# Kernel optimization log

Measured on AMD Instinct MI355X. Metric: run time of the kernel, lower is better.

Reference implementation:

```python
import jax, jax.numpy as jnp
import numpy as np


def setup_inputs() -> dict:
    key = jax.random.key(0)
    ks = jax.random.split(key, 8)
    B, C, H, W = 8, 256, 64, 64
    Cqk = C // 8
    x = jax.random.normal(ks[0], (B, C, H, W), dtype=jnp.float32)
    # 1x1 conv weights, stored as [out_ch, in_ch] (kernel is 1x1)
    Wq = jax.random.normal(ks[1], (Cqk, C), dtype=jnp.float32) * 0.02
    bq = jnp.zeros((Cqk,), dtype=jnp.float32)
    Wk = jax.random.normal(ks[2], (Cqk, C), dtype=jnp.float32) * 0.02
    bk = jnp.zeros((Cqk,), dtype=jnp.float32)
    Wv = jax.random.normal(ks[3], (C, C), dtype=jnp.float32) * 0.02
    bv = jnp.zeros((C,), dtype=jnp.float32)
    # gamma initialized to zero in the module; use small nonzero so grads flow through attention path meaningfully
    gamma = jnp.asarray([0.5], dtype=jnp.float32)
    return {"x": x, "Wq": Wq, "bq": bq, "Wk": Wk, "bk": bk, "Wv": Wv, "bv": bv, "gamma": gamma}


def reference(x, Wq, bq, Wk, bk, Wv, bv, gamma):
    B, C, H, W = x.shape
    N = H * W
    xf = x.reshape(B, C, N)  # [B, C, N]
    # 1x1 convs == channel-wise matmuls
    q = jnp.einsum('oc,bcn->bno', Wq, xf) + bq  # [B, N, Cqk]
    k = jnp.einsum('oc,bcn->bon', Wk, xf) + bk[None, :, None]  # [B, Cqk, N]
    v = jnp.einsum('oc,bcn->bon', Wv, xf) + bv[None, :, None]  # [B, C, N]
    energy = jnp.einsum('bnd,bdm->bnm', q, k)  # [B, N, N], unscaled as in original
    attn = jax.nn.softmax(energy, axis=-1)
    out = jnp.einsum('bcm,bnm->bcn', v, attn)  # out[:, :, n] = sum_m v[:, :, m] * attn[n, m]
    out = out.reshape(B, C, H, W)
    return gamma[0] * out + x
```

## Files before the change

### kernel.cpp

```cpp
#include <hip/hip_runtime.h>
#include <hip/hip_bf16.h>

#define NB 8
#define CH 256
#define NN 4096
#define CQK 32
#define LOG2E 1.4426950408889634f

typedef __attribute__((ext_vector_type(4))) float f32x4;
typedef __attribute__((ext_vector_type(8))) short bf16x8;
typedef unsigned short u16;

static __device__ __forceinline__ u16 f2bf(float f) {
  unsigned int u = __float_as_uint(f);
  unsigned int r = (u + 0x7fffu + ((u >> 16) & 1u)) >> 16;
  return (u16)r;
}

__global__ void prep_weights(const float* __restrict__ Wq, const float* __restrict__ bq,
                             const float* __restrict__ Wk, const float* __restrict__ bk,
                             const float* __restrict__ Wv,
                             u16* __restrict__ Wqkf, u16* __restrict__ Wvf,
                             float* __restrict__ bqk) {
  int i = blockIdx.x * 256 + threadIdx.x;
  int o = i >> 8, c = i & 255;
  int kk = c >> 5, g2 = (c >> 3) & 3, j = c & 7;
  if (o < 64) {
    float wv = (o < 32) ? Wq[o * 256 + c] * LOG2E : Wk[(o - 32) * 256 + c];
    Wqkf[((((o >> 4) * 8 + kk) * 4 + g2) * 16 + (o & 15)) * 8 + j] = f2bf(wv);
  }
  Wvf[((((o >> 4) * 8 + kk) * 4 + g2) * 16 + (o & 15)) * 8 + j] = f2bf(Wv[i]);
  if (i < 64) bqk[i] = (i < 32) ? bq[i] * LOG2E : bk[i - 32];
}

__global__ __launch_bounds__(256, 2) void fused_proj(
    const float* __restrict__ x, const u16* __restrict__ Wqkf,
    const u16* __restrict__ Wvf, const float* __restrict__ bqk,
    const float* __restrict__ bv,
    u16* __restrict__ qbuf, u16* __restrict__ kbuf, u16* __restrict__ vbuf) {
  __shared__ __align__(128) char xt[64 * 512];
  const int b = blockIdx.y, n0 = blockIdx.x * 64;
  const int tid = threadIdx.x, w = tid >> 6, l = tid & 63, g = l >> 4, lr = l & 15;
  const f32x4 fzero = {0.f, 0.f, 0.f, 0.f};

  {
    const int nl = l, cl = w;
    const float* xp = x + (size_t)b * CH * NN + n0 + nl;
    char* xrow = xt + nl * 512;
    const int swz = (nl & 15) << 4;
#pragma unroll
    for (int p = 0; p < 32; ++p) {
      const int c = p * 8 + cl * 2;
      float f0 = xp[(size_t)c * NN], f1 = xp[(size_t)(c + 1) * NN];
      unsigned int pk = (unsigned int)f2bf(f0) | ((unsigned int)f2bf(f1) << 16);
      *(unsigned int*)(xrow + ((c * 2) ^ swz)) = pk;
    }
  }
  __syncthreads();

  const int aswz = lr << 4;

  {
    f32x4 acc[4];
#pragma unroll
    for (int ct = 0; ct < 4; ++ct) acc[ct] = fzero;
#pragma unroll
    for (int kk = 0; kk < 8; ++kk) {
      bf16x8 af = *(const bf16x8*)(xt + (w * 16 + lr) * 512 + ((kk * 64 + g * 16) ^ aswz));
#pragma unroll
      for (int ct = 0; ct < 4; ++ct) {
        bf16x8 bf = *(const bf16x8*)(Wqkf + (size_t)(((ct * 8 + kk) * 4 + g) * 16 + lr) * 8);
        acc[ct] = __builtin_amdgcn_mfma_f32_16x16x32_bf16(af, bf, acc[ct], 0, 0, 0);
      }
    }
#pragma unroll
    for (int ct = 0; ct < 4; ++ct) {
      const int col = ct * 16 + lr;
      const float bc = bqk[col];
#pragma unroll
      for (int r = 0; r < 4; ++r) {
        const int row = n0 + w * 16 + g * 4 + r;
        u16 h = f2bf(acc[ct][r] + bc);
        if (col < 32) qbuf[((size_t)(b * NN + row)) * 32 + col] = h;
        else          kbuf[((size_t)(b * NN + row)) * 32 + (col - 32)] = h;
      }
    }
  }

  {
    f32x4 vacc[4][4];
#pragma unroll
    for (int ct = 0; ct < 4; ++ct)
#pragma unroll
      for (int mt = 0; mt < 4; ++mt) vacc[ct][mt] = fzero;
#pragma unroll
    for (int kk = 0; kk < 8; ++kk) {
      bf16x8 bfm[4];
#pragma unroll
      for (int mt = 0; mt < 4; ++mt)
        bfm[mt] = *(const bf16x8*)(xt + (mt * 16 + lr) * 512 + ((kk * 64 + g * 16) ^ aswz));
#pragma unroll
      for (int ct = 0; ct < 4; ++ct) {
        bf16x8 af = *(const bf16x8*)(Wvf + (size_t)((((w * 4 + ct) * 8 + kk) * 4 + g) * 16 + lr) * 8);
#pragma unroll
        for (int mt = 0; mt < 4; ++mt)
          vacc[ct][mt] = __builtin_amdgcn_mfma_f32_16x16x32_bf16(af, bfm[mt], vacc[ct][mt], 0, 0, 0);
      }
    }
#pragma unroll
    for (int ct = 0; ct < 4; ++ct) {
#pragma unroll
      for (int mt = 0; mt < 4; ++mt) {
        const int m = n0 + mt * 16 + lr;
#pragma unroll
        for (int r = 0; r < 4; ++r) {
          const int ch = w * 64 + ct * 16 + g * 4 + r;
          vbuf[((size_t)(b * 128 + (m >> 5)) * 256 + ch) * 32 + (m & 31)] = f2bf(vacc[ct][mt][r] + bv[ch]);
        }
      }
    }
  }
}

#define KLOAD(t, sub) (*(const bf16x8*)(kp + (size_t)((((t) & 63) * 64) + (sub) * 16) * 32))
#define VLOAD(mg, ct) (*(const bf16x8*)(vp + (size_t)((mg) & 127) * 8192 + (ct) * 512))

#define EXPP(S, PW, MASK) {                                                                   \
  float e0 = __builtin_amdgcn_exp2f(S[0]);                                                    \
  float e1 = __builtin_amdgcn_exp2f(S[1]);                                                    \
  float e2 = __builtin_amdgcn_exp2f(S[2]);                                                    \
  float e3 = __builtin_amdgcn_exp2f(S[3]);                                                    \
  lsum += (MASK) * ((e0 + e1) + (e2 + e3));                                                   \
  PW.x = __builtin_amdgcn_perm(__float_as_uint(e1) + 0x8000u, __float_as_uint(e0) + 0x8000u, 0x07060302u); \
  PW.y = __builtin_amdgcn_perm(__float_as_uint(e3) + 0x8000u, __float_as_uint(e2) + 0x8000u, 0x07060302u); \
}

#define PBAR() do {                                  \
  __builtin_amdgcn_sched_barrier(0);                 \
  asm volatile("s_waitcnt lgkmcnt(0)");              \
  __builtin_amdgcn_s_barrier();                      \
  __builtin_amdgcn_sched_barrier(0);                 \
} while (0)

#define PVPHASE(BUF, V0, V1, V2, V3) {                                                        \
  const char* prb = (const char*)Pb + (BUF) * 16384;                                          \
  char* pdst = (char*)Pb + ((BUF) ^ 1) * 16384 + prow * 128;                                  \
  *(uint2*)(pdst + ((0 * 32 + g * 8) ^ wswz)) = pw0;                                          \
  *(uint2*)(pdst + ((1 * 32 + g * 8) ^ wswz)) = pw1;                                          \
  *(uint2*)(pdst + ((2 * 32 + g * 8) ^ wswz)) = pw2;                                          \
  *(uint2*)(pdst + ((3 * 32 + g * 8) ^ wswz)) = pw3;                                          \
  __builtin_amdgcn_s_setprio(1);                                                              \
  _Pragma("unroll")                                                                           \
  for (int nt = 0; nt < 8; ++nt) {                                                            \
    const int row = nt * 16 + lr;                                                             \
    const int rs = (row & 7) << 4;                                                            \
    bf16x8 pa0 = *(const bf16x8*)(prb + row * 128 + ((g * 16) ^ rs));                         \
    bf16x8 pa1 = *(const bf16x8*)(prb + row * 128 + ((64 + g * 16) ^ rs));                    \
    oacc[nt][0] = __builtin_amdgcn_mfma_f32_16x16x32_bf16(V0, pa0, oacc[nt][0], 0, 0, 0);     \
    oacc[nt][1] = __builtin_amdgcn_mfma_f32_16x16x32_bf16(V1, pa0, oacc[nt][1], 0, 0, 0);     \
    oacc[nt][0] = __builtin_amdgcn_mfma_f32_16x16x32_bf16(V2, pa1, oacc[nt][0], 0, 0, 0);     \
    oacc[nt][1] = __builtin_amdgcn_mfma_f32_16x16x32_bf16(V3, pa1, oacc[nt][1], 0, 0, 0);     \
  }                                                                                           \
  __builtin_amdgcn_s_setprio(0);                                                              \
}

__global__ __launch_bounds__(512, 2) void attn_fused(
    const u16* __restrict__ qb, const u16* __restrict__ kbuf,
    const u16* __restrict__ vbuf, const float* __restrict__ x,
    const float* __restrict__ gamma_p, float* __restrict__ out) {
  __shared__ __align__(128) char Pb[2][128 * 128];
  __shared__ float lpart[8][16];

  const int b = blockIdx.x;
  const int n0 = blockIdx.y * 128;
  const int tid = threadIdx.x, w = tid >> 6, l = tid & 63, g = l >> 4, lr = l & 15;
  const float gamma0 = gamma_p[0];
  const f32x4 fzero = {0.f, 0.f, 0.f, 0.f};

  bf16x8 qf = *(const bf16x8*)(qb + ((size_t)b * NN + n0 + w * 16 + lr) * 32 + g * 8);

  const u16* kp = kbuf + (size_t)b * (NN * 32) + (size_t)lr * 32 + g * 8;
  const u16* vp = vbuf + (size_t)b * 1048576 + (size_t)(w * 32 + lr) * 32 + g * 8;

  f32x4 oacc[8][2];
#pragma unroll
  for (int nt = 0; nt < 8; ++nt)
#pragma unroll
    for (int ct = 0; ct < 2; ++ct) oacc[nt][ct] = fzero;
  float lsum = 0.f;

  const int prow = w * 16 + lr;
  const int wswz = (prow & 7) << 4;

  bf16x8 kA0 = KLOAD(0, 0), kA1 = KLOAD(0, 1), kA2 = KLOAD(0, 2), kA3 = KLOAD(0, 3);
  bf16x8 vA0 = VLOAD(0, 0), vA1 = VLOAD(0, 1), vA2 = VLOAD(1, 0), vA3 = VLOAD(1, 1);
  bf16x8 kB0 = KLOAD(1, 0), kB1 = KLOAD(1, 1), kB2 = KLOAD(1, 2), kB3 = KLOAD(1, 3);
  bf16x8 vB0, vB1, vB2, vB3;
  uint2 pw0, pw1, pw2, pw3;
  {
    f32x4 s0 = __builtin_amdgcn_mfma_f32_16x16x32_bf16(kA0, qf, fzero, 0, 0, 0);
    f32x4 s1 = __builtin_amdgcn_mfma_f32_16x16x32_bf16(kA1, qf, fzero, 0, 0, 0);
    f32x4 s2 = __builtin_amdgcn_mfma_f32_16x16x32_bf16(kA2, qf, fzero, 0, 0, 0);
    f32x4 s3 = __builtin_amdgcn_mfma_f32_16x16x32_bf16(kA3, qf, fzero, 0, 0, 0);
    EXPP(s0, pw0, 1.0f); EXPP(s1, pw1, 1.0f); EXPP(s2, pw2, 1.0f); EXPP(s3, pw3, 1.0f);
    char* pdst = (char*)Pb + prow * 128;
    *(uint2*)(pdst + ((0 * 32 + g * 8) ^ wswz)) = pw0;
    *(uint2*)(pdst + ((1 * 32 + g * 8) ^ wswz)) = pw1;
    *(uint2*)(pdst + ((2 * 32 + g * 8) ^ wswz)) = pw2;
    *(uint2*)(pdst + ((3 * 32 + g * 8) ^ wswz)) = pw3;
  }

  for (int it2 = 0; it2 < 32; ++it2) {
    {
      const int tn = 2 * it2 + 1;
      f32x4 s0 = __builtin_amdgcn_mfma_f32_16x16x32_bf16(kB0, qf, fzero, 0, 0, 0);
      f32x4 s1 = __builtin_amdgcn_mfma_f32_16x16x32_bf16(kB1, qf, fzero, 0, 0, 0);
      f32x4 s2 = __builtin_amdgcn_mfma_f32_16x16x32_bf16(kB2, qf, fzero, 0, 0, 0);
      f32x4 s3 = __builtin_amdgcn_mfma_f32_16x16x32_bf16(kB3, qf, fzero, 0, 0, 0);
      kA0 = KLOAD(tn + 1, 0); kA1 = KLOAD(tn + 1, 1); kA2 = KLOAD(tn + 1, 2); kA3 = KLOAD(tn + 1, 3);
      vB0 = VLOAD(2 * tn, 0); vB1 = VLOAD(2 * tn, 1);
      vB2 = VLOAD(2 * tn + 1, 0); vB3 = VLOAD(2 * tn + 1, 1);
      EXPP(s0, pw0, 1.0f); EXPP(s1, pw1, 1.0f); EXPP(s2, pw2, 1.0f); EXPP(s3, pw3, 1.0f);
      PBAR();
      PVPHASE(0, vA0, vA1, vA2, vA3);
    }
    {
      const int tn = 2 * it2 + 2;
      const float tmask = (it2 < 31) ? 1.0f : 0.0f;
      f32x4 s0 = __builtin_amdgcn_mfma_f32_16x16x32_bf16(kA0, qf, fzero, 0, 0, 0);
      f32x4 s1 = __builtin_amdgcn_mfma_f32_16x16x32_bf16(kA1, qf, fzero, 0, 0, 0);
      f32x4 s2 = __builtin_amdgcn_mfma_f32_16x16x32_bf16(kA2, qf, fzero, 0, 0, 0);
      f32x4 s3 = __builtin_amdgcn_mfma_f32_16x16x32_bf16(kA3, qf, fzero, 0, 0, 0);
      kB0 = KLOAD(tn + 1, 0); kB1 = KLOAD(tn + 1, 1); kB2 = KLOAD(tn + 1, 2); kB3 = KLOAD(tn + 1, 3);
      vA0 = VLOAD(2 * tn, 0); vA1 = VLOAD(2 * tn, 1);
      vA2 = VLOAD(2 * tn + 1, 0); vA3 = VLOAD(2 * tn + 1, 1);
      EXPP(s0, pw0, tmask); EXPP(s1, pw1, tmask); EXPP(s2, pw2, tmask); EXPP(s3, pw3, tmask);
      PBAR();
      PVPHASE(1, vB0, vB1, vB2, vB3);
    }
  }

  lsum += __shfl_xor(lsum, 16);
  lsum += __shfl_xor(lsum, 32);
  if (l < 16) lpart[w][lr] = lsum;
  __syncthreads();

  const size_t bbase = (size_t)b * CH * NN;
#pragma unroll
  for (int nt = 0; nt < 8; ++nt) {
    const float linv = 1.f / lpart[nt][lr];
    const int ncol = n0 + nt * 16 + lr;
#pragma unroll
    for (int ct = 0; ct < 2; ++ct) {
      const int cbase = w * 32 + ct * 16 + g * 4;
#pragma unroll
      for (int r = 0; r < 4; ++r) {
        const size_t off = bbase + (size_t)(cbase + r) * NN + ncol;
        out[off] = gamma0 * (oacc[nt][ct][r] * linv) + x[off];
      }
    }
  }
}

extern "C" void kernel_launch(void* const* d_in, const int* in_sizes, int n_in,
                              void* d_out, int out_size, void* d_ws, size_t ws_size,
                              hipStream_t stream) {
  const float* x     = (const float*)d_in[0];
  const float* Wq    = (const float*)d_in[1];
  const float* bq    = (const float*)d_in[2];
  const float* Wk    = (const float*)d_in[3];
  const float* bk    = (const float*)d_in[4];
  const float* Wv    = (const float*)d_in[5];
  const float* bv    = (const float*)d_in[6];
  const float* gamma = (const float*)d_in[7];
  float* out = (float*)d_out;

  char* ws = (char*)d_ws;
  u16*   qbuf = (u16*)(ws);
  u16*   kbuf = (u16*)(ws + 2097152);
  u16*   vbuf = (u16*)(ws + 4194304);
  u16*   Wqkf = (u16*)(ws + 20971520);
  u16*   Wvf  = (u16*)(ws + 21004288);
  float* bqk  = (float*)(ws + 21135360);

  prep_weights<<<256, 256, 0, stream>>>(Wq, bq, Wk, bk, Wv, Wqkf, Wvf, bqk);
  fused_proj<<<dim3(64, 8), 256, 0, stream>>>(x, Wqkf, Wvf, bqk, bv, qbuf, kbuf, vbuf);
  attn_fused<<<dim3(8, 32), 512, 0, stream>>>(qbuf, kbuf, vbuf, x, gamma, out);
}
```

Measured before the change: 109.8 us.

## Keep P in registers by permuting K layout, dropping LDS round-trip in attention

Reorders the key rows in the projection output so that the S=QK^T MFMA output fragment lines up with the B-operand layout of the PV MFMA. The exp'd probabilities can then be fed straight from registers, and the shared-memory P buffer and per-iteration block barriers go away. Each wave now owns 16 queries across all 256 channels, with 256-thread blocks on a 64x8 grid. The change removes LDS traffic and synchronisation, but every wave now streams the full V tile from global memory or cache, which raises global load pressure and register use.

```diff
diff --git a/kernel.cpp b/kernel.cpp
--- a/kernel.cpp
+++ b/kernel.cpp
@@ -81,8 +81,14 @@
       for (int r = 0; r < 4; ++r) {
         const int row = n0 + w * 16 + g * 4 + r;
         u16 h = f2bf(acc[ct][r] + bc);
-        if (col < 32) qbuf[((size_t)(b * NN + row)) * 32 + col] = h;
-        else          kbuf[((size_t)(b * NN + row)) * 32 + (col - 32)] = h;
+        if (col < 32) {
+          qbuf[((size_t)(b * NN + row)) * 32 + col] = h;
+        } else {
+          const int tile = row >> 6, mm = row & 63;
+          const int ct2 = 2 * ((mm >> 2) & 1) + ((mm >> 5) & 1);
+          const int rho = ct2 * 16 + ((mm >> 3) & 3) * 4 + (mm & 3);
+          kbuf[((size_t)(b * NN + tile * 64 + rho)) * 32 + (col - 32)] = h;
+        }
       }
     }
   }
@@ -123,7 +129,7 @@
 }
 
 #define KLOAD(t, sub) (*(const bf16x8*)(kp + (size_t)((((t) & 63) * 64) + (sub) * 16) * 32))
-#define VLOAD(mg, ct) (*(const bf16x8*)(vp + (size_t)((mg) & 127) * 8192 + (ct) * 512))
+#define VLOAD(mg, c) (*(const bf16x8*)(vp + (size_t)((mg) & 127) * 8192 + (c) * 512))
 
 #define EXPP(S, PW, MASK) {                                                                   \
   float e0 = __builtin_amdgcn_exp2f(S[0]);                                                    \
@@ -135,129 +141,95 @@
   PW.y = __builtin_amdgcn_perm(__float_as_uint(e3) + 0x8000u, __float_as_uint(e2) + 0x8000u, 0x07060302u); \
 }
 
-#define PBAR() do {                                  \
-  __builtin_amdgcn_sched_barrier(0);                 \
-  asm volatile("s_waitcnt lgkmcnt(0)");              \
-  __builtin_amdgcn_s_barrier();                      \
-  __builtin_amdgcn_sched_barrier(0);                 \
-} while (0)
-
-#define PVPHASE(BUF, V0, V1, V2, V3) {                                                        \
-  const char* prb = (const char*)Pb + (BUF) * 16384;                                          \
-  char* pdst = (char*)Pb + ((BUF) ^ 1) * 16384 + prow * 128;                                  \
-  *(uint2*)(pdst + ((0 * 32 + g * 8) ^ wswz)) = pw0;                                          \
-  *(uint2*)(pdst + ((1 * 32 + g * 8) ^ wswz)) = pw1;                                          \
-  *(uint2*)(pdst + ((2 * 32 + g * 8) ^ wswz)) = pw2;                                          \
-  *(uint2*)(pdst + ((3 * 32 + g * 8) ^ wswz)) = pw3;                                          \
-  __builtin_amdgcn_s_setprio(1);                                                              \
-  _Pragma("unroll")                                                                           \
-  for (int nt = 0; nt < 8; ++nt) {                                                            \
-    const int row = nt * 16 + lr;                                                             \
-    const int rs = (row & 7) << 4;                                                            \
-    bf16x8 pa0 = *(const bf16x8*)(prb + row * 128 + ((g * 16) ^ rs));                         \
-    bf16x8 pa1 = *(const bf16x8*)(prb + row * 128 + ((64 + g * 16) ^ rs));                    \
-    oacc[nt][0] = __builtin_amdgcn_mfma_f32_16x16x32_bf16(V0, pa0, oacc[nt][0], 0, 0, 0);     \
-    oacc[nt][1] = __builtin_amdgcn_mfma_f32_16x16x32_bf16(V1, pa0, oacc[nt][1], 0, 0, 0);     \
-    oacc[nt][0] = __builtin_amdgcn_mfma_f32_16x16x32_bf16(V2, pa1, oacc[nt][0], 0, 0, 0);     \
-    oacc[nt][1] = __builtin_amdgcn_mfma_f32_16x16x32_bf16(V3, pa1, oacc[nt][1], 0, 0, 0);     \
-  }                                                                                           \
-  __builtin_amdgcn_s_setprio(0);                                                              \
-}
-
-__global__ __launch_bounds__(512, 2) void attn_fused(
+__global__ __launch_bounds__(256, 2) void attn_fused(
     const u16* __restrict__ qb, const u16* __restrict__ kbuf,
     const u16* __restrict__ vbuf, const float* __restrict__ x,
     const float* __restrict__ gamma_p, float* __restrict__ out) {
-  __shared__ __align__(128) char Pb[2][128 * 128];
-  __shared__ float lpart[8][16];
-
-  const int b = blockIdx.x;
-  const int n0 = blockIdx.y * 128;
+  const int b = blockIdx.y;
   const int tid = threadIdx.x, w = tid >> 6, l = tid & 63, g = l >> 4, lr = l & 15;
+  const int qt = blockIdx.x * 4 + w;
   const float gamma0 = gamma_p[0];
   const f32x4 fzero = {0.f, 0.f, 0.f, 0.f};
 
-  bf16x8 qf = *(const bf16x8*)(qb + ((size_t)b * NN + n0 + w * 16 + lr) * 32 + g * 8);
+  bf16x8 qf = *(const bf16x8*)(qb + ((size_t)b * NN + qt * 16 + lr) * 32 + g * 8);
 
   const u16* kp = kbuf + (size_t)b * (NN * 32) + (size_t)lr * 32 + g * 8;
-  const u16* vp = vbuf + (size_t)b * 1048576 + (size_t)(w * 32 + lr) * 32 + g * 8;
-
-  f32x4 oacc[8][2];
-#pragma unroll
-  for (int nt = 0; nt < 8; ++nt)
-#pragma unroll
-    for (int ct = 0; ct < 2; ++ct) oacc[nt][ct] = fzero;
+  const u16* vp = vbuf + (size_t)b * 1048576 + (size_t)lr * 32 + g * 8;
+
+  f32x4 oacc[16];
+#pragma unroll
+  for (int c = 0; c < 16; ++c) oacc[c] = fzero;
   float lsum = 0.f;
 
-  const int prow = w * 16 + lr;
-  const int wswz = (prow & 7) << 4;
-
-  bf16x8 kA0 = KLOAD(0, 0), kA1 = KLOAD(0, 1), kA2 = KLOAD(0, 2), kA3 = KLOAD(0, 3);
-  bf16x8 vA0 = VLOAD(0, 0), vA1 = VLOAD(0, 1), vA2 = VLOAD(1, 0), vA3 = VLOAD(1, 1);
-  bf16x8 kB0 = KLOAD(1, 0), kB1 = KLOAD(1, 1), kB2 = KLOAD(1, 2), kB3 = KLOAD(1, 3);
-  bf16x8 vB0, vB1, vB2, vB3;
+  bf16x8 kf0 = KLOAD(0, 0), kf1 = KLOAD(0, 1), kf2 = KLOAD(0, 2), kf3 = KLOAD(0, 3);
   uint2 pw0, pw1, pw2, pw3;
   {
-    f32x4 s0 = __builtin_amdgcn_mfma_f32_16x16x32_bf16(kA0, qf, fzero, 0, 0, 0);
-    f32x4 s1 = __builtin_amdgcn_mfma_f32_16x16x32_bf16(kA1, qf, fzero, 0, 0, 0);
-    f32x4 s2 = __builtin_amdgcn_mfma_f32_16x16x32_bf16(kA2, qf, fzero, 0, 0, 0);
-    f32x4 s3 = __builtin_amdgcn_mfma_f32_16x16x32_bf16(kA3, qf, fzero, 0, 0, 0);
+    f32x4 s0 = __builtin_amdgcn_mfma_f32_16x16x32_bf16(kf0, qf, fzero, 0, 0, 0);
+    f32x4 s1 = __builtin_amdgcn_mfma_f32_16x16x32_bf16(kf1, qf, fzero, 0, 0, 0);
+    f32x4 s2 = __builtin_amdgcn_mfma_f32_16x16x32_bf16(kf2, qf, fzero, 0, 0, 0);
+    f32x4 s3 = __builtin_amdgcn_mfma_f32_16x16x32_bf16(kf3, qf, fzero, 0, 0, 0);
     EXPP(s0, pw0, 1.0f); EXPP(s1, pw1, 1.0f); EXPP(s2, pw2, 1.0f); EXPP(s3, pw3, 1.0f);
-    char* pdst = (char*)Pb + prow * 128;
-    *(uint2*)(pdst + ((0 * 32 + g * 8) ^ wswz)) = pw0;
-    *(uint2*)(pdst + ((1 * 32 + g * 8) ^ wswz)) = pw1;
-    *(uint2*)(pdst + ((2 * 32 + g * 8) ^ wswz)) = pw2;
-    *(uint2*)(pdst + ((3 * 32 + g * 8) ^ wswz)) = pw3;
-  }
-
-  for (int it2 = 0; it2 < 32; ++it2) {
-    {
-      const int tn = 2 * it2 + 1;
-      f32x4 s0 = __builtin_amdgcn_mfma_f32_16x16x32_bf16(kB0, qf, fzero, 0, 0, 0);
-      f32x4 s1 = __builtin_amdgcn_mfma_f32_16x16x32_bf16(kB1, qf, fzero, 0, 0, 0);
-      f32x4 s2 = __builtin_amdgcn_mfma_f32_16x16x32_bf16(kB2, qf, fzero, 0, 0, 0);
-      f32x4 s3 = __builtin_amdgcn_mfma_f32_16x16x32_bf16(kB3, qf, fzero, 0, 0, 0);
-      kA0 = KLOAD(tn + 1, 0); kA1 = KLOAD(tn + 1, 1); kA2 = KLOAD(tn + 1, 2); kA3 = KLOAD(tn + 1, 3);
-      vB0 = VLOAD(2 * tn, 0); vB1 = VLOAD(2 * tn, 1);
-      vB2 = VLOAD(2 * tn + 1, 0); vB3 = VLOAD(2 * tn + 1, 1);
-      EXPP(s0, pw0, 1.0f); EXPP(s1, pw1, 1.0f); EXPP(s2, pw2, 1.0f); EXPP(s3, pw3, 1.0f);
-      PBAR();
-      PVPHASE(0, vA0, vA1, vA2, vA3);
-    }
-    {
-      const int tn = 2 * it2 + 2;
-      const float tmask = (it2 < 31) ? 1.0f : 0.0f;
-      f32x4 s0 = __builtin_amdgcn_mfma_f32_16x16x32_bf16(kA0, qf, fzero, 0, 0, 0);
-      f32x4 s1 = __builtin_amdgcn_mfma_f32_16x16x32_bf16(kA1, qf, fzero, 0, 0, 0);
-      f32x4 s2 = __builtin_amdgcn_mfma_f32_16x16x32_bf16(kA2, qf, fzero, 0, 0, 0);
-      f32x4 s3 = __builtin_amdgcn_mfma_f32_16x16x32_bf16(kA3, qf, fzero, 0, 0, 0);
-      kB0 = KLOAD(tn + 1, 0); kB1 = KLOAD(tn + 1, 1); kB2 = KLOAD(tn + 1, 2); kB3 = KLOAD(tn + 1, 3);
-      vA0 = VLOAD(2 * tn, 0); vA1 = VLOAD(2 * tn, 1);
-      vA2 = VLOAD(2 * tn + 1, 0); vA3 = VLOAD(2 * tn + 1, 1);
-      EXPP(s0, pw0, tmask); EXPP(s1, pw1, tmask); EXPP(s2, pw2, tmask); EXPP(s3, pw3, tmask);
-      PBAR();
-      PVPHASE(1, vB0, vB1, vB2, vB3);
-    }
+  }
+  kf0 = KLOAD(1, 0); kf1 = KLOAD(1, 1); kf2 = KLOAD(1, 2); kf3 = KLOAD(1, 3);
+  bf16x8 vA[8], vB[8];
+#pragma unroll
+  for (int c = 0; c < 8; ++c) vA[c] = VLOAD(0, c);
+#pragma unroll
+  for (int c = 0; c < 8; ++c) vB[c] = VLOAD(0, 8 + c);
+
+  for (int t = 0; t < 64; ++t) {
+    uint4 u0; u0.x = pw0.x; u0.y = pw0.y; u0.z = pw2.x; u0.w = pw2.y;
+    uint4 u1; u1.x = pw1.x; u1.y = pw1.y; u1.z = pw3.x; u1.w = pw3.y;
+    bf16x8 pf0 = __builtin_bit_cast(bf16x8, u0);
+    bf16x8 pf1 = __builtin_bit_cast(bf16x8, u1);
+
+    f32x4 s0 = __builtin_amdgcn_mfma_f32_16x16x32_bf16(kf0, qf, fzero, 0, 0, 0);
+    f32x4 s1 = __builtin_amdgcn_mfma_f32_16x16x32_bf16(kf1, qf, fzero, 0, 0, 0);
+    f32x4 s2 = __builtin_amdgcn_mfma_f32_16x16x32_bf16(kf2, qf, fzero, 0, 0, 0);
+    f32x4 s3 = __builtin_amdgcn_mfma_f32_16x16x32_bf16(kf3, qf, fzero, 0, 0, 0);
+    kf0 = KLOAD(t + 2, 0); kf1 = KLOAD(t + 2, 1); kf2 = KLOAD(t + 2, 2); kf3 = KLOAD(t + 2, 3);
+
+#pragma unroll
+    for (int c = 0; c < 8; ++c)
+      oacc[c] = __builtin_amdgcn_mfma_f32_16x16x32_bf16(vA[c], pf0, oacc[c], 0, 0, 0);
+#pragma unroll
+    for (int c = 0; c < 8; ++c) vA[c] = VLOAD(2 * t + 1, c);
+
+    const float tmask = (t < 63) ? 1.0f : 0.0f;
+    EXPP(s0, pw0, tmask); EXPP(s1, pw1, tmask); EXPP(s2, pw2, tmask); EXPP(s3, pw3, tmask);
+
+#pragma unroll
+    for (int c = 0; c < 8; ++c)
+      oacc[8 + c] = __builtin_amdgcn_mfma_f32_16x16x32_bf16(vB[c], pf0, oacc[8 + c], 0, 0, 0);
+#pragma unroll
+    for (int c = 0; c < 8; ++c) vB[c] = VLOAD(2 * t + 1, 8 + c);
+
+#pragma unroll
+    for (int c = 0; c < 8; ++c)
+      oacc[c] = __builtin_amdgcn_mfma_f32_16x16x32_bf16(vA[c], pf1, oacc[c], 0, 0, 0);
+#pragma unroll
+    for (int c = 0; c < 8; ++c) vA[c] = VLOAD(2 * t + 2, c);
+
+#pragma unroll
+    for (int c = 0; c < 8; ++c)
+      oacc[8 + c] = __builtin_amdgcn_mfma_f32_16x16x32_bf16(vB[c], pf1, oacc[8 + c], 0, 0, 0);
+#pragma unroll
+    for (int c = 0; c < 8; ++c) vB[c] = VLOAD(2 * t + 2, 8 + c);
   }
 
   lsum += __shfl_xor(lsum, 16);
   lsum += __shfl_xor(lsum, 32);
-  if (l < 16) lpart[w][lr] = lsum;
-  __syncthreads();
+  const float linv = 1.f / lsum;
 
   const size_t bbase = (size_t)b * CH * NN;
-#pragma unroll
-  for (int nt = 0; nt < 8; ++nt) {
-    const float linv = 1.f / lpart[nt][lr];
-    const int ncol = n0 + nt * 16 + lr;
-#pragma unroll
-    for (int ct = 0; ct < 2; ++ct) {
-      const int cbase = w * 32 + ct * 16 + g * 4;
-#pragma unroll
-      for (int r = 0; r < 4; ++r) {
-        const size_t off = bbase + (size_t)(cbase + r) * NN + ncol;
-        out[off] = gamma0 * (oacc[nt][ct][r] * linv) + x[off];
-      }
+  const int n = qt * 16 + lr;
+#pragma unroll
+  for (int c = 0; c < 16; ++c) {
+#pragma unroll
+    for (int r = 0; r < 4; ++r) {
+      const int ch = c * 16 + g * 4 + r;
+      const size_t off = bbase + (size_t)ch * NN + n;
+      out[off] = gamma0 * (oacc[c][r] * linv) + x[off];
     }
   }
 }
@@ -285,5 +257,5 @@
 
   prep_weights<<<256, 256, 0, stream>>>(Wq, bq, Wk, bk, Wv, Wqkf, Wvf, bqk);
   fused_proj<<<dim3(64, 8), 256, 0, stream>>>(x, Wqkf, Wvf, bqk, bv, qbuf, kbuf, vbuf);
-  attn_fused<<<dim3(8, 32), 512, 0, stream>>>(qbuf, kbuf, vbuf, x, gamma, out);
-}
+  attn_fused<<<dim3(64, 8), 256, 0, stream>>>(qbuf, kbuf, vbuf, x, gamma, out);
+}
```

Measured after the change: 291.6 us. 2.65x slower.
